# Performance work log

Hardware: AMD Instinct MI355X
Metric: run time of the kernel (lower is better)

Reference implementation:

```python
import jax, jax.numpy as jnp
import numpy as np

N_NODES = 20000
DEG = 16
T_IN = 12
T_OUT = 24
N_HEADS = 4
N_CH = 4
BATCH = 2


def setup_inputs() -> dict:
    key = jax.random.key(0)
    k1, k2, k3, k4 = jax.random.split(key, 4)
    # unique directed edges: (i, (i+d) % N) for d in 1..DEG, plus self loops
    src = jnp.repeat(jnp.arange(N_NODES, dtype=jnp.int64), DEG)
    offs = jnp.tile(jnp.arange(1, DEG + 1, dtype=jnp.int64), N_NODES)
    dst = (src + offs) % N_NODES
    loops = jnp.arange(N_NODES, dtype=jnp.int64)
    d_edges = jnp.concatenate([
        jnp.stack([src, dst], axis=1),
        jnp.stack([loops, loops], axis=1),
    ], axis=0)  # (E, 2), E = N*DEG + N
    E = d_edges.shape[0]
    x = jax.random.normal(k1, (BATCH, T_IN, N_NODES, N_CH), dtype=jnp.float32)
    d_ew = jax.random.uniform(k2, (E, N_HEADS), dtype=jnp.float32)
    # shrink: Linear(t_in*n_heads -> T-t_in)
    fan_in = T_IN * N_HEADS
    bound = 1.0 / np.sqrt(fan_in)
    W = jax.random.uniform(k3, (T_OUT - T_IN, fan_in), minval=-bound, maxval=bound, dtype=jnp.float32)
    b = jax.random.uniform(k4, (T_OUT - T_IN,), minval=-bound, maxval=bound, dtype=jnp.float32)
    return {"x": x, "d_ew": d_ew, "W": W, "b": b, "d_edges": d_edges}


def reference(x, d_ew, W, b, d_edges):
    # x: (B, t, N, C); d_ew: (E, H); d_edges: (E, 2)
    node_i = d_edges[:, 0]
    node_j = d_edges[:, 1]
    B, t, N, C = x.shape
    # gather source node features per edge -> (E, B, t, C)
    x_src = jnp.moveaxis(x[:, :, node_i, :], 2, 0)
    # messages: (E, B, t, H, C)
    msg = d_ew[:, None, None, :, None] * x_src[:, :, :, None, :]
    # scatter-add into destination nodes (equivalent to the dense N x N holder sum)
    agg = jax.ops.segment_sum(msg, node_j, num_segments=N)  # (N, B, t, H, C)
    y = jnp.moveaxis(agg, 0, 2)                              # (B, t, N, H, C)
    # permute(0,2,4,1,3) -> (B, N, C, t, H), flatten (t, H)
    y = jnp.transpose(y, (0, 2, 4, 1, 3)).reshape(B, N, C, t * d_ew.shape[1])
    y = jax.nn.relu(jnp.einsum('bncf,of->bnco', y, W) + b)   # (B, N, C, T-t)
    y = jnp.transpose(y, (0, 3, 1, 2))                       # (B, T-t, N, C)
    return jnp.concatenate([x, y], axis=1)                   # (B, T, N, C)
```

## Files before the change

kernel.cpp:

```cpp
#include <hip/hip_runtime.h>

namespace {
constexpr int NN  = 20000;
constexpr int DEG = 16;
constexpr int NB  = 2;
constexpr int ESELF  = NN * DEG;
constexpr int TILE   = 32;
constexpr int NTILES = NN / TILE;
constexpr int WN     = 48;
}

__device__ __forceinline__ void pk_fma_blo(float2& d, float2 a, float2 b) {
    asm("v_pk_fma_f32 %0, %1, %2, %0 op_sel:[0,0,0] op_sel_hi:[1,0,1]"
        : "+v"(d) : "v"(a), "v"(b));
}
__device__ __forceinline__ void pk_fma_bhi(float2& d, float2 a, float2 b) {
    asm("v_pk_fma_f32 %0, %1, %2, %0 op_sel:[0,1,0] op_sel_hi:[1,1,1]"
        : "+v"(d) : "v"(a), "v"(b));
}

__global__ __launch_bounds__(256) void gnn_fused(
    const float* __restrict__ x,
    const float* __restrict__ ew,
    const float* __restrict__ W,
    const float* __restrict__ bias,
    float* __restrict__ out)
{
    __shared__ __align__(16) float x_lds[NB * 12 * WN * 4];
    __shared__ float2 red[NB][64][13];

    const int tid = threadIdx.x;

    int bid = blockIdx.x;
    {
        const int q = NTILES >> 3, r = NTILES & 7;
        const int xcd = bid & 7, idx = bid >> 3;
        bid = (xcd < r ? xcd * (q + 1) : r * (q + 1) + (xcd - r) * q) + idx;
    }
    const int n0 = bid * TILE;

    const int c2 = tid & 1;
    const int nl = (tid >> 1) & 31;
    const int tg = (tid >> 6) & 1;
    const int b  = tid >> 7;
    const int t0 = __builtin_amdgcn_readfirstlane(((tid >> 6) & 1) * 6);
    const int n  = n0 + nl;

    const float* xr = x + ((size_t)b * 12 * NN + n) * 4 + c2 * 2;
    float2 xself[6];
#pragma unroll
    for (int j = 0; j < 6; ++j)
        xself[j] = *(const float2*)&xr[(size_t)(t0 + j) * NN * 4];
    const float4 es = *(const float4*)(ew + (size_t)(ESELF + n) * 4);

#pragma unroll
    for (int i = 0; i < 5; ++i) {
        if (i < 4 || tid < 128) {
            const int idx4 = i * 256 + tid;
            const int bb = idx4 / 576;
            const int r  = idx4 - bb * 576;
            const int t  = r / WN;
            const int wi = r - t * WN;
            int s = n0 - 16 + wi; s += (s >> 31) & NN;
            const float* src = x + ((size_t)bb * 12 + t) * NN * 4 + (size_t)s * 4;
            float* dst = x_lds + (size_t)(i * 256 + (tid & ~63)) * 4;
            __builtin_amdgcn_global_load_lds(
                (const __attribute__((address_space(1))) void*)src,
                (__attribute__((address_space(3))) void*)dst, 16, 0, 0);
        }
    }
    __syncthreads();

    const size_t ob = ((size_t)b * 24 * NN + n) * 4 + c2 * 2;
#pragma unroll
    for (int j = 0; j < 6; ++j)
        *(float2*)&out[ob + (size_t)(t0 + j) * NN * 4] = xself[j];

    const float* xbl = x_lds + (size_t)b * 12 * WN * 4;
    const float4* ew4 = (const float4*)ew;
    float2 agg[6][4] = {};
#pragma unroll
    for (int k = 0; k < DEG; ++k) {
        int s = n - 1 - k; s += (s >> 31) & NN;
        const float4 e4 = ew4[s * DEG + k];
        const int wi = nl + 15 - k;
        const float2 e01 = {e4.x, e4.y}, e23 = {e4.z, e4.w};
#pragma unroll
        for (int j = 0; j < 6; ++j) {
            const float2 xv = *(const float2*)&xbl[((t0 + j) * WN + wi) * 4 + c2 * 2];
            pk_fma_blo(agg[j][0], xv, e01);
            pk_fma_bhi(agg[j][1], xv, e01);
            pk_fma_blo(agg[j][2], xv, e23);
            pk_fma_bhi(agg[j][3], xv, e23);
        }
    }
    {
        const float2 e01 = {es.x, es.y}, e23 = {es.z, es.w};
#pragma unroll
        for (int j = 0; j < 6; ++j) {
            pk_fma_blo(agg[j][0], xself[j], e01);
            pk_fma_bhi(agg[j][1], xself[j], e01);
            pk_fma_blo(agg[j][2], xself[j], e23);
            pk_fma_bhi(agg[j][3], xself[j], e23);
        }
    }

    float2 y2[12];
#pragma unroll
    for (int o = 0; o < 12; ++o) {
        float2 acc = {0.f, 0.f};
#pragma unroll
        for (int j = 0; j < 6; ++j) {
            const float* Wr = W + o * 48 + (t0 + j) * 4;
#pragma unroll
            for (int h = 0; h < 4; ++h) {
                acc.x = fmaf(Wr[h], agg[j][h].x, acc.x);
                acc.y = fmaf(Wr[h], agg[j][h].y, acc.y);
            }
        }
        y2[o] = acc;
    }

    const int lane = tid & 63;
    if (tg == 1) {
#pragma unroll
        for (int o = 0; o < 12; ++o) red[b][lane][o] = y2[o];
    }
    __syncthreads();
    if (tg == 0) {
#pragma unroll
        for (int o = 0; o < 12; ++o) {
            const float2 p = red[b][lane][o];
            const float bo = bias[o];
            float2 v = {fmaxf(y2[o].x + p.x + bo, 0.f),
                        fmaxf(y2[o].y + p.y + bo, 0.f)};
            *(float2*)&out[ob + (size_t)(12 + o) * NN * 4] = v;
        }
    }
}

extern "C" void kernel_launch(void* const* d_in, const int* in_sizes, int n_in,
                              void* d_out, int out_size, void* d_ws, size_t ws_size,
                              hipStream_t stream) {
    const float* x    = (const float*)d_in[0];
    const float* ew   = (const float*)d_in[1];
    const float* W    = (const float*)d_in[2];
    const float* bias = (const float*)d_in[3];
    float* out = (float*)d_out;

    hipLaunchKernelGGL(gnn_fused, dim3(NTILES), dim3(256), 0, stream,
                       x, ew, W, bias, out);
}
```

Before: 17.72 us.

## Stage edge weights in LDS via async copy and split final reduction across halves

Edge weights for the 48-node window are loaded into shared memory with global_load_lds using an XOR swizzle, replacing the 16 per-thread strided global float4 loads in the aggregation loop. Self features are now read from the already-staged x tile instead of a separate global load. The cross-half reduction is balanced so each half writes six outputs and reduces the other six, rather than one half doing all twelve. This adds about 12KB of LDS per block, which may lower occupancy, and the swizzle indexing must match the copy layout.

```diff
diff --git a/kernel.cpp b/kernel.cpp
--- a/kernel.cpp
+++ b/kernel.cpp
@@ -27,6 +27,7 @@
     float* __restrict__ out)
 {
     __shared__ __align__(16) float x_lds[NB * 12 * WN * 4];
+    __shared__ __align__(16) float ew_lds[WN * 16 * 4];
     __shared__ float2 red[NB][64][13];
 
     const int tid = threadIdx.x;
@@ -46,11 +47,6 @@
     const int t0 = __builtin_amdgcn_readfirstlane(((tid >> 6) & 1) * 6);
     const int n  = n0 + nl;
 
-    const float* xr = x + ((size_t)b * 12 * NN + n) * 4 + c2 * 2;
-    float2 xself[6];
-#pragma unroll
-    for (int j = 0; j < 6; ++j)
-        xself[j] = *(const float2*)&xr[(size_t)(t0 + j) * NN * 4];
     const float4 es = *(const float4*)(ew + (size_t)(ESELF + n) * 4);
 
 #pragma unroll
@@ -69,21 +65,36 @@
                 (__attribute__((address_space(3))) void*)dst, 16, 0, 0);
         }
     }
+#pragma unroll
+    for (int i = 0; i < 3; ++i) {
+        const int slot = i * 256 + tid;
+        const int wi   = slot >> 4;
+        const int kk   = slot & 15;
+        const int ks   = kk ^ (wi & 15);
+        int s = n0 - 16 + wi; s += (s >> 31) & NN;
+        const float* src = ew + (size_t)(s * DEG + ks) * 4;
+        float* dst = ew_lds + (size_t)(i * 256 + (tid & ~63)) * 4;
+        __builtin_amdgcn_global_load_lds(
+            (const __attribute__((address_space(1))) void*)src,
+            (__attribute__((address_space(3))) void*)dst, 16, 0, 0);
+    }
     __syncthreads();
 
     const size_t ob = ((size_t)b * 24 * NN + n) * 4 + c2 * 2;
+    const float* xbl = x_lds + (size_t)b * 12 * WN * 4;
+    float2 xself[6];
 #pragma unroll
-    for (int j = 0; j < 6; ++j)
+    for (int j = 0; j < 6; ++j) {
+        xself[j] = *(const float2*)&xbl[((t0 + j) * WN + nl + 16) * 4 + c2 * 2];
         *(float2*)&out[ob + (size_t)(t0 + j) * NN * 4] = xself[j];
+    }
 
-    const float* xbl = x_lds + (size_t)b * 12 * WN * 4;
-    const float4* ew4 = (const float4*)ew;
     float2 agg[6][4] = {};
 #pragma unroll
     for (int k = 0; k < DEG; ++k) {
-        int s = n - 1 - k; s += (s >> 31) & NN;
-        const float4 e4 = ew4[s * DEG + k];
         const int wi = nl + 15 - k;
+        const float4 e4 =
+            *(const float4*)&ew_lds[(wi * 16 + (k ^ (wi & 15))) * 4];
         const float2 e01 = {e4.x, e4.y}, e23 = {e4.z, e4.w};
 #pragma unroll
         for (int j = 0; j < 6; ++j) {
@@ -122,19 +133,22 @@
     }
 
     const int lane = tid & 63;
-    if (tg == 1) {
+    {
+        const int obase = tg ? 0 : 6;
 #pragma unroll
-        for (int o = 0; o < 12; ++o) red[b][lane][o] = y2[o];
+        for (int o = 0; o < 6; ++o) red[b][lane][obase + o] = y2[obase + o];
     }
     __syncthreads();
-    if (tg == 0) {
+    {
+        const int obase = tg ? 6 : 0;
 #pragma unroll
-        for (int o = 0; o < 12; ++o) {
-            const float2 p = red[b][lane][o];
-            const float bo = bias[o];
-            float2 v = {fmaxf(y2[o].x + p.x + bo, 0.f),
-                        fmaxf(y2[o].y + p.y + bo, 0.f)};
-            *(float2*)&out[ob + (size_t)(12 + o) * NN * 4] = v;
+        for (int o = 0; o < 6; ++o) {
+            const int oo = obase + o;
+            const float2 p = red[b][lane][oo];
+            const float bo = bias[oo];
+            float2 v = {fmaxf(y2[oo].x + p.x + bo, 0.f),
+                        fmaxf(y2[oo].y + p.y + bo, 0.f)};
+            *(float2*)&out[ob + (size_t)(12 + oo) * NN * 4] = v;
         }
     }
 }
```

Result: slower. 21.27 us (+20.0%).

## Enlarge node tile to 160 per batch-specific workgroup and read self features from LDS

Applied to the files above, without the earlier changes.

Workgroups now each handle one batch and a 160-node tile with 640 threads, where before one workgroup covered both batches for 32 nodes. This shrinks the 16-node halo overhead per staged tile. Self-node features now come from the staged LDS window rather than a separate global load. The reduction buffer reuses the x_lds space, which needs an extra barrier. The larger blocks mean fewer workgroups (250 instead of 625), which may lower occupancy and latency hiding on a 256-CU device.

```diff
diff --git a/kernel.cpp b/kernel.cpp
--- a/kernel.cpp
+++ b/kernel.cpp
@@ -3,11 +3,12 @@
 namespace {
 constexpr int NN  = 20000;
 constexpr int DEG = 16;
-constexpr int NB  = 2;
-constexpr int ESELF  = NN * DEG;
-constexpr int TILE   = 32;
+constexpr int ESELF = NN * DEG;
+constexpr int TILE  = 160;
 constexpr int NTILES = NN / TILE;
-constexpr int WN     = 48;
+constexpr int NWG    = 2 * NTILES;
+constexpr int WN     = TILE + 16;
+constexpr int NROWS  = 12 * WN;
 }
 
 __device__ __forceinline__ void pk_fma_blo(float2& d, float2 a, float2 b) {
@@ -19,51 +20,37 @@
         : "+v"(d) : "v"(a), "v"(b));
 }
 
-__global__ __launch_bounds__(256) void gnn_fused(
+__global__ __launch_bounds__(640) void gnn_fused(
     const float* __restrict__ x,
     const float* __restrict__ ew,
     const float* __restrict__ W,
     const float* __restrict__ bias,
     float* __restrict__ out)
 {
-    __shared__ __align__(16) float x_lds[NB * 12 * WN * 4];
-    __shared__ float2 red[NB][64][13];
+    __shared__ __align__(16) float x_lds[NROWS * 4];
 
     const int tid = threadIdx.x;
 
     int bid = blockIdx.x;
     {
-        const int q = NTILES >> 3, r = NTILES & 7;
+        const int q = NWG >> 3, r = NWG & 7;
         const int xcd = bid & 7, idx = bid >> 3;
         bid = (xcd < r ? xcd * (q + 1) : r * (q + 1) + (xcd - r) * q) + idx;
     }
-    const int n0 = bid * TILE;
-
-    const int c2 = tid & 1;
-    const int nl = (tid >> 1) & 31;
-    const int tg = (tid >> 6) & 1;
-    const int b  = tid >> 7;
-    const int t0 = __builtin_amdgcn_readfirstlane(((tid >> 6) & 1) * 6);
-    const int n  = n0 + nl;
-
-    const float* xr = x + ((size_t)b * 12 * NN + n) * 4 + c2 * 2;
-    float2 xself[6];
-#pragma unroll
-    for (int j = 0; j < 6; ++j)
-        xself[j] = *(const float2*)&xr[(size_t)(t0 + j) * NN * 4];
-    const float4 es = *(const float4*)(ew + (size_t)(ESELF + n) * 4);
+    const int b  = bid & 1;
+    const int n0 = (bid >> 1) * TILE;
 
 #pragma unroll
-    for (int i = 0; i < 5; ++i) {
-        if (i < 4 || tid < 128) {
-            const int idx4 = i * 256 + tid;
-            const int bb = idx4 / 576;
-            const int r  = idx4 - bb * 576;
+    for (int i = 0; i < 4; ++i) {
+        if (i < 3 || tid < NROWS - 3 * 640) {
+            const int r  = i * 640 + tid;
             const int t  = r / WN;
             const int wi = r - t * WN;
-            int s = n0 - 16 + wi; s += (s >> 31) & NN;
-            const float* src = x + ((size_t)bb * 12 + t) * NN * 4 + (size_t)s * 4;
-            float* dst = x_lds + (size_t)(i * 256 + (tid & ~63)) * 4;
+            int s = n0 - 16 + wi;
+            s += (s >> 31) & NN;
+            if (s >= NN) s -= NN;
+            const float* src = x + ((size_t)(b * 12 + t) * NN + s) * 4;
+            float* dst = x_lds + (size_t)(i * 640 + (tid & ~63)) * 4;
             __builtin_amdgcn_global_load_lds(
                 (const __attribute__((address_space(1))) void*)src,
                 (__attribute__((address_space(3))) void*)dst, 16, 0, 0);
@@ -71,13 +58,23 @@
     }
     __syncthreads();
 
+    const int tg = (tid >= 320) ? 1 : 0;
+    const int u  = tid - tg * 320;
+    const int c2 = u & 1;
+    const int nl = u >> 1;
+    const int t0 = __builtin_amdgcn_readfirstlane(tg * 6);
+    const int n  = n0 + nl;
+
     const size_t ob = ((size_t)b * 24 * NN + n) * 4 + c2 * 2;
+    float2 xself[6];
 #pragma unroll
-    for (int j = 0; j < 6; ++j)
+    for (int j = 0; j < 6; ++j) {
+        xself[j] = *(const float2*)&x_lds[((t0 + j) * WN + nl + 16) * 4 + c2 * 2];
         *(float2*)&out[ob + (size_t)(t0 + j) * NN * 4] = xself[j];
+    }
 
-    const float* xbl = x_lds + (size_t)b * 12 * WN * 4;
     const float4* ew4 = (const float4*)ew;
+    const float4 es = ew4[ESELF + n];
     float2 agg[6][4] = {};
 #pragma unroll
     for (int k = 0; k < DEG; ++k) {
@@ -87,7 +84,7 @@
         const float2 e01 = {e4.x, e4.y}, e23 = {e4.z, e4.w};
 #pragma unroll
         for (int j = 0; j < 6; ++j) {
-            const float2 xv = *(const float2*)&xbl[((t0 + j) * WN + wi) * 4 + c2 * 2];
+            const float2 xv = *(const float2*)&x_lds[((t0 + j) * WN + wi) * 4 + c2 * 2];
             pk_fma_blo(agg[j][0], xv, e01);
             pk_fma_bhi(agg[j][1], xv, e01);
             pk_fma_blo(agg[j][2], xv, e23);
@@ -121,16 +118,17 @@
         y2[o] = acc;
     }
 
-    const int lane = tid & 63;
+    __syncthreads();
+    float2 (*red)[13] = (float2(*)[13])x_lds;
     if (tg == 1) {
 #pragma unroll
-        for (int o = 0; o < 12; ++o) red[b][lane][o] = y2[o];
+        for (int o = 0; o < 12; ++o) red[u][o] = y2[o];
     }
     __syncthreads();
     if (tg == 0) {
 #pragma unroll
         for (int o = 0; o < 12; ++o) {
-            const float2 p = red[b][lane][o];
+            const float2 p = red[u][o];
             const float bo = bias[o];
             float2 v = {fmaxf(y2[o].x + p.x + bo, 0.f),
                         fmaxf(y2[o].y + p.y + bo, 0.f)};
@@ -148,6 +146,6 @@
     const float* bias = (const float*)d_in[3];
     float* out = (float*)d_out;
 
-    hipLaunchKernelGGL(gnn_fused, dim3(NTILES), dim3(256), 0, stream,
+    hipLaunchKernelGGL(gnn_fused, dim3(NWG), dim3(640), 0, stream,
                        x, ew, W, bias, out);
 }
```

Measured after the change: 16.78 us. 1.06x faster.
